# Performance work log

Measured on AMD Instinct MI355X. Metric: run time of the kernel, lower is better.

## Reference

```python
import jax, jax.numpy as jnp
import numpy as np


def setup_inputs() -> dict:
    key = jax.random.key(0)
    k1, k2, k3 = jax.random.split(key, 3)
    n, p2, w2, c_kv, topk = 32, 49, 64, 256, 4
    r_idx = jax.random.randint(k1, (n, p2, topk), 0, p2, dtype=jnp.int64)
    r_weight = jax.random.uniform(k2, (n, p2, topk), dtype=jnp.float32)
    kv = jax.random.normal(k3, (n, p2, w2, c_kv), dtype=jnp.float32)
    return {"r_idx": r_idx, "r_weight": r_weight, "kv": kv}


def reference(r_idx, r_weight, kv):
    # KVGather with mul_weight='soft'
    # kv: (n, p2, w2, c), r_idx/r_weight: (n, p2, topk)
    # out[b, i, k, w, c] = r_weight[b, i, k] * kv[b, r_idx[b, i, k], w, c]
    idx = r_idx[:, :, :, None, None]                 # (n, p2, topk, 1, 1)
    topk_kv = jnp.take_along_axis(kv[:, None], idx, axis=2)  # (n, p2, topk, w2, c)
    return r_weight[:, :, :, None, None] * topk_kv
```

## Files before the change

kernel.cpp:

```cpp
#include <hip/hip_runtime.h>

constexpr int N    = 32;
constexpr int P2   = 49;
constexpr int TOPK = 4;
constexpr int W2   = 64;
constexpr int CKV  = 256;
constexpr int ROW  = W2 * CKV;
constexpr int ROW4 = ROW / 4;
constexpr int G    = N * P2 * TOPK;
constexpr int HALF4 = ROW4 / 2;
constexpr int NBLK = G * 2;

typedef float floatx4 __attribute__((ext_vector_type(4)));

__global__ __launch_bounds__(256)
void kv_gather_scale(const int* __restrict__ r_idx,
                     const float* __restrict__ r_weight,
                     const float* __restrict__ kv,
                     float* __restrict__ out) {
    const int bid  = blockIdx.x;
    const int g    = bid >> 1;
    const int half = bid & 1;
    const int b    = g / (P2 * TOPK);

    const int   src = r_idx[g];
    const float w   = r_weight[g];

    const int off = half * HALF4;
    const floatx4* __restrict__ s =
        (const floatx4*)(kv + (size_t)(b * P2 + src) * ROW) + off;
    floatx4* __restrict__ d = (floatx4*)(out + (size_t)g * ROW) + off;

    #pragma unroll
    for (int i = threadIdx.x; i < HALF4; i += 256) {
        d[i] = s[i] * w;
    }
}

extern "C" void kernel_launch(void* const* d_in, const int* in_sizes, int n_in,
                              void* d_out, int out_size, void* d_ws, size_t ws_size,
                              hipStream_t stream) {
    const int*   r_idx    = (const int*)d_in[0];
    const float* r_weight = (const float*)d_in[1];
    const float* kv       = (const float*)d_in[2];
    float*       out      = (float*)d_out;

    kv_gather_scale<<<NBLK, 256, 0, stream>>>(r_idx, r_weight, kv, out);
}
```

Baseline: 112.6 us.

## Convert gather-scale kernel to persistent grid with prefetched indices

The launch shrinks from one block per half-row to a fixed grid of 1792 blocks, each looping over several half-rows with a stride of the grid size. The next iteration's index and weight are loaded before the current copy so their latency overlaps the streaming. This is meant to cut block launch and scheduling overhead and hide the dependent index load. In exchange, fewer blocks are in flight, which could reduce memory-level parallelism, and it relies on the total count dividing evenly by 1792.

```diff
diff --git a/kernel.cpp b/kernel.cpp
--- a/kernel.cpp
+++ b/kernel.cpp
@@ -9,7 +9,9 @@
 constexpr int ROW4 = ROW / 4;
 constexpr int G    = N * P2 * TOPK;
 constexpr int HALF4 = ROW4 / 2;
-constexpr int NBLK = G * 2;
+constexpr int NH   = G * 2;
+constexpr int NBLK = 1792;
+constexpr int ITERS = NH / NBLK;
 
 typedef float floatx4 __attribute__((ext_vector_type(4)));
 
@@ -18,22 +20,34 @@
                      const float* __restrict__ r_weight,
                      const float* __restrict__ kv,
                      float* __restrict__ out) {
-    const int bid  = blockIdx.x;
-    const int g    = bid >> 1;
-    const int half = bid & 1;
-    const int b    = g / (P2 * TOPK);
+    const floatx4* __restrict__ kv4  = (const floatx4*)kv;
+    floatx4* __restrict__       out4 = (floatx4*)out;
 
-    const int   src = r_idx[g];
-    const float w   = r_weight[g];
+    int   h   = blockIdx.x;
+    int   g   = h >> 1;
+    int   src = r_idx[g];
+    float w   = r_weight[g];
 
-    const int off = half * HALF4;
-    const floatx4* __restrict__ s =
-        (const floatx4*)(kv + (size_t)(b * P2 + src) * ROW) + off;
-    floatx4* __restrict__ d = (floatx4*)(out + (size_t)g * ROW) + off;
+    #pragma unroll 1
+    for (int it = 0; it < ITERS; ++it) {
+        const int hn = h + NBLK;
+        const int gn = hn >> 1;
+        int   srcn = 0;
+        float wn   = 0.f;
+        if (it + 1 < ITERS) { srcn = r_idx[gn]; wn = r_weight[gn]; }
 
-    #pragma unroll
-    for (int i = threadIdx.x; i < HALF4; i += 256) {
-        d[i] = s[i] * w;
+        const int b   = g / (P2 * TOPK);
+        const int off = (h & 1) * HALF4;
+        const floatx4* __restrict__ s =
+            kv4 + (size_t)(b * P2 + src) * ROW4 + off;
+        floatx4* __restrict__ d = out4 + (size_t)g * ROW4 + off;
+
+        #pragma unroll
+        for (int i = threadIdx.x; i < HALF4; i += 256) {
+            d[i] = s[i] * w;
+        }
+
+        h = hn; g = gn; src = srcn; w = wn;
     }
 }
 
```

After: 122.8 us. +9.1%, slower.
